# Optimization experiments

Measured on AMD Instinct MI355X. Metric: run time of the kernel, lower is better.

The kernel has to match this reference:

```python
import jax, jax.numpy as jnp
import numpy as np

H = 16
D_MODEL = 1024
D_K = D_MODEL // H
B, S = 4, 2048


def setup_inputs() -> dict:
    key = jax.random.key(0)
    ks = jax.random.split(key, 12)
    s = 1.0 / np.sqrt(D_MODEL)
    inp = {
        "q": jax.random.normal(ks[0], (B, S, D_MODEL), jnp.float32),
        "k": jax.random.normal(ks[1], (B, S, D_MODEL), jnp.float32),
        "v": jax.random.normal(ks[2], (B, S, D_MODEL), jnp.float32),
        "mask": jnp.ones((B, S, S), jnp.int32),
        "Wq": jax.random.normal(ks[3], (D_MODEL, D_MODEL), jnp.float32) * s,
        "bq": jnp.zeros((D_MODEL,), jnp.float32),
        "Wk": jax.random.normal(ks[4], (D_MODEL, D_MODEL), jnp.float32) * s,
        "bk": jnp.zeros((D_MODEL,), jnp.float32),
        "Wv": jax.random.normal(ks[5], (D_MODEL, D_MODEL), jnp.float32) * s,
        "bv": jnp.zeros((D_MODEL,), jnp.float32),
        "Wo": jax.random.normal(ks[6], (D_MODEL, D_MODEL), jnp.float32) * s,
        "bo": jnp.zeros((D_MODEL,), jnp.float32),
    }
    return inp


def _shape_heads(x):
    # [B, S, d_model] -> [B, H, S, d_k]
    b, s, _ = x.shape
    return x.reshape(b, s, H, D_K).transpose(0, 2, 1, 3)


def reference(q, k, v, mask, Wq, bq, Wk, bk, Wv, bv, Wo, bo):
    qh = _shape_heads(q @ Wq + bq)  # [B,H,S,dk]
    kh = _shape_heads(k @ Wk + bk)
    vh = _shape_heads(v @ Wv + bv)
    scores = jnp.einsum("bhqd,bhkd->bhqk", qh, kh) / jnp.sqrt(jnp.float32(D_K))
    scores = jnp.where(mask[:, None, :, :] == 0, jnp.float32(-1e9), scores)
    attn = jax.nn.softmax(scores, axis=-1)  # dropout = identity (eval)
    ctx = jnp.einsum("bhqk,bhkd->bhqd", attn, vh)
    concat = ctx.transpose(0, 2, 1, 3).reshape(q.shape[0], -1, D_MODEL)
    output = concat @ Wo + bo
    return output, attn
```

## Files before the change

kernel.cpp:

```cpp
#include <hip/hip_runtime.h>

#define NH     16
#define SEQ    2048
#define DMODEL 1024
#define DK     64
#define NB     4

typedef __attribute__((ext_vector_type(8))) short short8v;
typedef __attribute__((ext_vector_type(4))) short short4v;
typedef __attribute__((ext_vector_type(4))) float f32x4;

#define EXP_SC 0.18033688011f

__device__ __forceinline__ short f2bf(float x) {
  unsigned u = __float_as_uint(x);
  unsigned r = (u + 0x7FFFu + ((u >> 16) & 1u)) >> 16;
  return (short)r;
}
__device__ __forceinline__ float bf2f(short b) {
  return __uint_as_float(((unsigned)(unsigned short)b) << 16);
}

typedef const __attribute__((address_space(1))) unsigned int* gas_t;
typedef __attribute__((address_space(3))) unsigned int* las_t;
__device__ __forceinline__ void glds16(const void* g, void* l) {
  __builtin_amdgcn_global_load_lds((gas_t)g, (las_t)l, 16, 0, 0);
}

__device__ __forceinline__ void stage_tile(const void* grow0, int gpitchB,
                                           void* ltile, int wid, int lane) {
#pragma unroll
  for (int i = 0; i < 2; ++i) {
    const int row = i * 32 + wid * 8 + (lane >> 3);
    const int srccol = ((lane & 7) * 16) ^ ((lane >> 3) << 4);
    const char* src = reinterpret_cast<const char*>(grow0) + (size_t)row * gpitchB + srccol;
    char* dst = reinterpret_cast<char*>(ltile) + i * 4096 + wid * 1024;
    glds16(src, dst);
  }
}

__device__ __forceinline__ short8v ldfrag(const short* base, int row, int colByte) {
  return *reinterpret_cast<const short8v*>(
      reinterpret_cast<const char*>(base) + row * 128 + (colByte ^ ((row & 7) << 4)));
}
__device__ __forceinline__ void st8b(short* base, int row, int colByte, short4v v) {
  *reinterpret_cast<short4v*>(
      reinterpret_cast<char*>(base) + row * 128 + (colByte ^ ((row & 7) << 4))) = v;
}

__device__ __forceinline__ void stPf4(float* base, int row, int colByte, float4 v) {
  *reinterpret_cast<float4*>(
      reinterpret_cast<char*>(base) + row * 256 + (colByte ^ ((row & 7) << 4))) = v;
}
__device__ __forceinline__ float4 ldPf4(const float* base, int row, int colByte) {
  return *reinterpret_cast<const float4*>(
      reinterpret_cast<const char*>(base) + row * 256 + (colByte ^ ((row & 7) << 4)));
}

__global__ __launch_bounds__(256) void pack_mask_kernel(
    const int* __restrict__ mask, unsigned long long* __restrict__ bits)
{
  const int t = threadIdx.x;
  const size_t chunk = (size_t)blockIdx.x * 4 + (t >> 6);
  const int lane = t & 63;
  const int m = mask[chunk * 64 + lane];
  const unsigned long long b = __ballot(m != 0);
  if (lane == 0) bits[chunk] = b;
}

__global__ __launch_bounds__(256) void convert_f32_bf16_kernel(
    const float* __restrict__ in, short* __restrict__ out)
{
  const int idx = blockIdx.x * 256 + threadIdx.x;
  const float4 x0 = *reinterpret_cast<const float4*>(&in[(size_t)idx * 8]);
  const float4 x1 = *reinterpret_cast<const float4*>(&in[(size_t)idx * 8 + 4]);
  short8v o;
  o[0] = f2bf(x0.x); o[1] = f2bf(x0.y); o[2] = f2bf(x0.z); o[3] = f2bf(x0.w);
  o[4] = f2bf(x1.x); o[5] = f2bf(x1.y); o[6] = f2bf(x1.z); o[7] = f2bf(x1.w);
  *reinterpret_cast<short8v*>(&out[(size_t)idx * 8]) = o;
}

__global__ __launch_bounds__(256) void transpose_w_kernel(
    const float* __restrict__ W, short* __restrict__ WT)
{
  __shared__ short T[64][80];
  const int t  = threadIdx.x;
  const int k0 = blockIdx.x * 64;
  const int n0 = blockIdx.y * 64;

  const int kl = t >> 2, nc = (t & 3) * 16;
#pragma unroll
  for (int i = 0; i < 4; ++i) {
    const float4 x = *reinterpret_cast<const float4*>(&W[(size_t)(k0 + kl) * DMODEL + n0 + nc + i * 4]);
    T[nc + i * 4 + 0][kl] = f2bf(x.x);
    T[nc + i * 4 + 1][kl] = f2bf(x.y);
    T[nc + i * 4 + 2][kl] = f2bf(x.z);
    T[nc + i * 4 + 3][kl] = f2bf(x.w);
  }
  __syncthreads();
  const int nl = t >> 2, kc = (t & 3) * 16;
#pragma unroll
  for (int i = 0; i < 2; ++i) {
    const short8v y = *reinterpret_cast<const short8v*>(&T[nl][kc + i * 8]);
    *reinterpret_cast<short8v*>(&WT[(size_t)(n0 + nl) * DMODEL + k0 + kc + i * 8]) = y;
  }
}

__global__ __launch_bounds__(256) void transpose_w_hilo_kernel(
    const float* __restrict__ W, short* __restrict__ WTh, short* __restrict__ WTl)
{
  __shared__ short Th[64][80];
  __shared__ short Tl[64][80];
  const int t  = threadIdx.x;
  const int k0 = blockIdx.x * 64;
  const int n0 = blockIdx.y * 64;

  const int kl = t >> 2, nc = (t & 3) * 16;
#pragma unroll
  for (int i = 0; i < 4; ++i) {
    const float4 x = *reinterpret_cast<const float4*>(&W[(size_t)(k0 + kl) * DMODEL + n0 + nc + i * 4]);
    const float xv[4] = {x.x, x.y, x.z, x.w};
#pragma unroll
    for (int j = 0; j < 4; ++j) {
      const short hi = f2bf(xv[j]);
      const short lo = f2bf(xv[j] - bf2f(hi));
      Th[nc + i * 4 + j][kl] = hi;
      Tl[nc + i * 4 + j][kl] = lo;
    }
  }
  __syncthreads();
  const int nl = t >> 2, kc = (t & 3) * 16;
#pragma unroll
  for (int i = 0; i < 2; ++i) {
    const short8v yh = *reinterpret_cast<const short8v*>(&Th[nl][kc + i * 8]);
    const short8v yl = *reinterpret_cast<const short8v*>(&Tl[nl][kc + i * 8]);
    *reinterpret_cast<short8v*>(&WTh[(size_t)(n0 + nl) * DMODEL + k0 + kc + i * 8]) = yh;
    *reinterpret_cast<short8v*>(&WTl[(size_t)(n0 + nl) * DMODEL + k0 + kc + i * 8]) = yl;
  }
}

__global__ __launch_bounds__(256) void proj_mfma_kernel(
    const short* __restrict__ A,
    const short* __restrict__ BT,
    const float* __restrict__ bias,
    short* __restrict__ out)
{
  __shared__ short As[128 * 64];
  __shared__ short Bs[128 * 64];

  const int t = threadIdx.x, lane = t & 63, wid = t >> 6;
  const int g = lane >> 4, r15 = lane & 15;
  const int m0 = blockIdx.x * 128, n0 = blockIdx.y * 128;
  const int wm = (wid >> 1) * 64, wn = (wid & 1) * 64;

  f32x4 acc[4][4];
#pragma unroll
  for (int i = 0; i < 4; ++i)
#pragma unroll
    for (int j = 0; j < 4; ++j) acc[i][j] = (f32x4){0.f, 0.f, 0.f, 0.f};

  for (int k0 = 0; k0 < DMODEL; k0 += 64) {
    __syncthreads();
    stage_tile(A + (size_t)m0 * DMODEL + k0, DMODEL * 2, As, wid, lane);
    stage_tile(A + (size_t)(m0 + 64) * DMODEL + k0, DMODEL * 2, As + 64 * 64, wid, lane);
    stage_tile(BT + (size_t)n0 * DMODEL + k0, DMODEL * 2, Bs, wid, lane);
    stage_tile(BT + (size_t)(n0 + 64) * DMODEL + k0, DMODEL * 2, Bs + 64 * 64, wid, lane);
    __syncthreads();

#pragma unroll
    for (int w = 0; w < 2; ++w) {
      short8v a[4], b[4];
#pragma unroll
      for (int i = 0; i < 4; ++i) a[i] = ldfrag(As, wm + i * 16 + r15, w * 64 + g * 16);
#pragma unroll
      for (int j = 0; j < 4; ++j) b[j] = ldfrag(Bs, wn + j * 16 + r15, w * 64 + g * 16);
#pragma unroll
      for (int i = 0; i < 4; ++i)
#pragma unroll
        for (int j = 0; j < 4; ++j)
          acc[i][j] = __builtin_amdgcn_mfma_f32_16x16x32_bf16(a[i], b[j], acc[i][j], 0, 0, 0);
    }
  }

#pragma unroll
  for (int j = 0; j < 4; ++j) {
    const int n = n0 + wn + j * 16 + r15;
    const int hh = n >> 6, dd = n & 63;
    const float bv = bias[n];
#pragma unroll
    for (int i = 0; i < 4; ++i) {
#pragma unroll
      for (int reg = 0; reg < 4; ++reg) {
        const int m = m0 + wm + i * 16 + g * 4 + reg;
        const int bb = m >> 11, ss = m & 2047;
        out[((size_t)(bb * NH + hh) * SEQ + ss) * DK + dd] = f2bf(acc[i][j][reg] + bv);
      }
    }
  }
}

__global__ __launch_bounds__(256) void outproj_mfma_kernel(
    const short* __restrict__ Ahp, const short* __restrict__ Alp,
    const short* __restrict__ BTh, const short* __restrict__ BTl,
    const float* __restrict__ bias, float* __restrict__ out)
{
  __shared__ short Ah[128 * 64];
  __shared__ short Al[128 * 64];
  __shared__ short Bh[128 * 64];
  __shared__ short Bl[128 * 64];

  const int t = threadIdx.x, lane = t & 63, wid = t >> 6;
  const int g = lane >> 4, r15 = lane & 15;
  const int m0 = blockIdx.x * 128, n0 = blockIdx.y * 128;
  const int wm = (wid >> 1) * 64, wn = (wid & 1) * 64;

  f32x4 acc[4][4];
#pragma unroll
  for (int i = 0; i < 4; ++i)
#pragma unroll
    for (int j = 0; j < 4; ++j) acc[i][j] = (f32x4){0.f, 0.f, 0.f, 0.f};

  for (int k0 = 0; k0 < DMODEL; k0 += 64) {
    __syncthreads();
    stage_tile(Ahp + (size_t)m0 * DMODEL + k0, DMODEL * 2, Ah, wid, lane);
    stage_tile(Ahp + (size_t)(m0 + 64) * DMODEL + k0, DMODEL * 2, Ah + 64 * 64, wid, lane);
    stage_tile(Alp + (size_t)m0 * DMODEL + k0, DMODEL * 2, Al, wid, lane);
    stage_tile(Alp + (size_t)(m0 + 64) * DMODEL + k0, DMODEL * 2, Al + 64 * 64, wid, lane);
    stage_tile(BTh + (size_t)n0 * DMODEL + k0, DMODEL * 2, Bh, wid, lane);
    stage_tile(BTh + (size_t)(n0 + 64) * DMODEL + k0, DMODEL * 2, Bh + 64 * 64, wid, lane);
    stage_tile(BTl + (size_t)n0 * DMODEL + k0, DMODEL * 2, Bl, wid, lane);
    stage_tile(BTl + (size_t)(n0 + 64) * DMODEL + k0, DMODEL * 2, Bl + 64 * 64, wid, lane);
    __syncthreads();

#pragma unroll
    for (int w = 0; w < 2; ++w) {
      short8v ah[4], al[4];
#pragma unroll
      for (int i = 0; i < 4; ++i) {
        ah[i] = ldfrag(Ah, wm + i * 16 + r15, w * 64 + g * 16);
        al[i] = ldfrag(Al, wm + i * 16 + r15, w * 64 + g * 16);
      }
#pragma unroll
      for (int j = 0; j < 4; ++j) {
        const short8v bh = ldfrag(Bh, wn + j * 16 + r15, w * 64 + g * 16);
        const short8v bl = ldfrag(Bl, wn + j * 16 + r15, w * 64 + g * 16);
#pragma unroll
        for (int i = 0; i < 4; ++i) {
          acc[i][j] = __builtin_amdgcn_mfma_f32_16x16x32_bf16(ah[i], bh, acc[i][j], 0, 0, 0);
          acc[i][j] = __builtin_amdgcn_mfma_f32_16x16x32_bf16(ah[i], bl, acc[i][j], 0, 0, 0);
          acc[i][j] = __builtin_amdgcn_mfma_f32_16x16x32_bf16(al[i], bh, acc[i][j], 0, 0, 0);
        }
      }
    }
  }

#pragma unroll
  for (int j = 0; j < 4; ++j) {
    const int n = n0 + wn + j * 16 + r15;
    const float bv = bias[n];
#pragma unroll
    for (int i = 0; i < 4; ++i)
#pragma unroll
      for (int reg = 0; reg < 4; ++reg) {
        const int m = m0 + wm + i * 16 + g * 4 + reg;
        out[(size_t)m * DMODEL + n] = acc[i][j][reg] + bv;
      }
  }
}

__global__ __launch_bounds__(256) void transpose_v_kernel(
    const short* __restrict__ vhb, short* __restrict__ vT)
{
  __shared__ short T[64][72];
  const int t    = threadIdx.x;
  const int s0   = blockIdx.x * 64;
  const int head = blockIdx.y;
  const size_t ibase = (size_t)head * SEQ * DK;
  const size_t obase = (size_t)head * DK * SEQ;

  const int sl = t >> 2, d0 = (t & 3) * 16;
#pragma unroll
  for (int i = 0; i < 2; ++i) {
    const short8v x = *reinterpret_cast<const short8v*>(
        &vhb[ibase + (size_t)(s0 + sl) * DK + d0 + i * 8]);
#pragma unroll
    for (int j = 0; j < 8; ++j) T[d0 + i * 8 + j][sl] = x[j];
  }
  __syncthreads();
  const int dl = t >> 2, soff = (t & 3) * 16;
#pragma unroll
  for (int i = 0; i < 2; ++i) {
    const short8v y = *reinterpret_cast<const short8v*>(&T[dl][soff + i * 8]);
    *reinterpret_cast<short8v*>(&vT[obase + (size_t)dl * SEQ + s0 + soff + i * 8]) = y;
  }
}

__global__ __launch_bounds__(256) void flash_kernel(
    const short* __restrict__ qh, const short* __restrict__ kh,
    const short* __restrict__ vT, const unsigned long long* __restrict__ maskbits,
    short* __restrict__ ctxh, short* __restrict__ ctxl,
    float* __restrict__ linv_arr)
{
  __shared__ short Qs[64 * 64];
  __shared__ short Ks[64 * 64];
  __shared__ short VsT[64 * 64];
  __shared__ short Psb[64 * 64];

  const int t    = threadIdx.x;
  const int lane = t & 63;
  const int wid  = t >> 6;
  const int g    = lane >> 4;
  const int r15  = lane & 15;
  const int qbase = wid * 16;
  const int qrow  = qbase + r15;

  const int q0 = blockIdx.x * 64;
  const int h  = blockIdx.y;
  const int b  = blockIdx.z;

  const size_t headbase = ((size_t)(b * NH + h)) * SEQ * DK;
  const size_t vTbase   = ((size_t)(b * NH + h)) * DK * SEQ;
  const size_t mrow     = ((size_t)b * SEQ + (q0 + qrow)) * (SEQ / 64);

  stage_tile(qh + headbase + (size_t)q0 * DK, DK * 2, Qs, wid, lane);
  __syncthreads();

  const short8v bQ0 = ldfrag(Qs, qrow, g * 16);
  const short8v bQ1 = ldfrag(Qs, qrow, 64 + g * 16);

  float lsum = 0.f;
  f32x4 cacc[4];
#pragma unroll
  for (int i = 0; i < 4; ++i) cacc[i] = (f32x4){0.f, 0.f, 0.f, 0.f};

  for (int t64 = 0; t64 < 32; ++t64) {
    __syncthreads();
    stage_tile(kh + headbase + (size_t)t64 * 64 * DK, DK * 2, Ks, wid, lane);
    stage_tile(reinterpret_cast<const char*>(vT + vTbase + t64 * 64), SEQ * 2, VsT, wid, lane);
    __syncthreads();

    f32x4 acc[4];
#pragma unroll
    for (int t4 = 0; t4 < 4; ++t4) acc[t4] = (f32x4){0.f, 0.f, 0.f, 0.f};
#pragma unroll
    for (int t4 = 0; t4 < 4; ++t4) {
      const short8v aK0 = ldfrag(Ks, t4 * 16 + r15, g * 16);
      const short8v aK1 = ldfrag(Ks, t4 * 16 + r15, 64 + g * 16);
      acc[t4] = __builtin_amdgcn_mfma_f32_16x16x32_bf16(aK0, bQ0, acc[t4], 0, 0, 0);
      acc[t4] = __builtin_amdgcn_mfma_f32_16x16x32_bf16(aK1, bQ1, acc[t4], 0, 0, 0);
    }

    const unsigned long long mb = maskbits[mrow + t64];
#pragma unroll
    for (int t4 = 0; t4 < 4; ++t4) {
      const unsigned b4 = (unsigned)(mb >> (t4 * 16 + g * 4)) & 0xFu;
      short4v pk;
#pragma unroll
      for (int reg = 0; reg < 4; ++reg) {
        const float p = ((b4 >> reg) & 1u) ? exp2f(acc[t4][reg] * EXP_SC) : 0.f;
        lsum += p;
        pk[reg] = f2bf(p);
      }
      st8b(Psb, qrow, t4 * 32 + g * 8, pk);
    }

    {
      const short8v aP0 = ldfrag(Psb, qrow, g * 16);
      const short8v aP1 = ldfrag(Psb, qrow, 64 + g * 16);
#pragma unroll
      for (int dt = 0; dt < 4; ++dt) {
        const short8v bV0 = ldfrag(VsT, dt * 16 + r15, g * 16);
        const short8v bV1 = ldfrag(VsT, dt * 16 + r15, 64 + g * 16);
        cacc[dt] = __builtin_amdgcn_mfma_f32_16x16x32_bf16(aP0, bV0, cacc[dt], 0, 0, 0);
        cacc[dt] = __builtin_amdgcn_mfma_f32_16x16x32_bf16(aP1, bV1, cacc[dt], 0, 0, 0);
      }
    }
  }

  float l = lsum;
  l += __shfl_xor(l, 16);
  l += __shfl_xor(l, 32);
  const float linv = 1.0f / l;
  if (g == 0)
    linv_arr[(size_t)(b * NH + h) * SEQ + q0 + qrow] = linv;

  float linvr[4];
#pragma unroll
  for (int reg = 0; reg < 4; ++reg) linvr[reg] = __shfl(linv, g * 4 + reg);

#pragma unroll
  for (int dt = 0; dt < 4; ++dt)
#pragma unroll
    for (int reg = 0; reg < 4; ++reg) {
      const float x = cacc[dt][reg] * linvr[reg];
      const short hi = f2bf(x);
      const short lo = f2bf(x - bf2f(hi));
      const size_t off = (size_t)(b * SEQ + q0 + qbase + g * 4 + reg) * DMODEL
                       + h * DK + dt * 16 + r15;
      ctxh[off] = hi;
      ctxl[off] = lo;
    }
}

__global__ __launch_bounds__(256) void probs_kernel(
    const short* __restrict__ qh, const short* __restrict__ kh,
    const unsigned long long* __restrict__ maskbits,
    const float* __restrict__ linv_arr,
    float* __restrict__ attn_out)
{
  __shared__ short Qs[64 * 64];
  __shared__ short Ks[2][64 * 64];
  __shared__ float PsbF[64 * 64];

  const int t    = threadIdx.x;
  const int lane = t & 63;
  const int wid  = t >> 6;
  const int g    = lane >> 4;
  const int r15  = lane & 15;
  const int qbase = wid * 16;
  const int qrow  = qbase + r15;

  const int q0 = blockIdx.x * 64;
  const int h  = blockIdx.y;
  const int b  = blockIdx.z;

  const size_t headbase = ((size_t)(b * NH + h)) * SEQ * DK;
  const size_t attnbase = ((size_t)(b * NH + h)) * SEQ * SEQ;
  const size_t mrow     = ((size_t)b * SEQ + (q0 + qrow)) * (SEQ / 64);

  const float linv = linv_arr[(size_t)(b * NH + h) * SEQ + q0 + qrow];

  stage_tile(qh + headbase + (size_t)q0 * DK, DK * 2, Qs, wid, lane);
  stage_tile(kh + headbase, DK * 2, Ks[0], wid, lane);
  asm volatile("s_waitcnt vmcnt(0)" ::: "memory");
  __builtin_amdgcn_s_barrier();

  const short8v bQ0 = ldfrag(Qs, qrow, g * 16);
  const short8v bQ1 = ldfrag(Qs, qrow, 64 + g * 16);

  for (int t64 = 0; t64 < 32; ++t64) {
    const int cur = t64 & 1;
    if (t64 + 1 < 32)
      stage_tile(kh + headbase + (size_t)(t64 + 1) * 64 * DK, DK * 2,
                 Ks[cur ^ 1], wid, lane);
    __builtin_amdgcn_sched_barrier(0);

    f32x4 acc[4];
#pragma unroll
    for (int t4 = 0; t4 < 4; ++t4) acc[t4] = (f32x4){0.f, 0.f, 0.f, 0.f};
#pragma unroll
    for (int t4 = 0; t4 < 4; ++t4) {
      const short8v aK0 = ldfrag(Ks[cur], t4 * 16 + r15, g * 16);
      const short8v aK1 = ldfrag(Ks[cur], t4 * 16 + r15, 64 + g * 16);
      acc[t4] = __builtin_amdgcn_mfma_f32_16x16x32_bf16(aK0, bQ0, acc[t4], 0, 0, 0);
      acc[t4] = __builtin_amdgcn_mfma_f32_16x16x32_bf16(aK1, bQ1, acc[t4], 0, 0, 0);
    }

    const unsigned long long mb = maskbits[mrow + t64];
#pragma unroll
    for (int t4 = 0; t4 < 4; ++t4) {
      const unsigned b4 = (unsigned)(mb >> (t4 * 16 + g * 4)) & 0xFu;
      float4 pv;
      pv.x = (b4 & 1u) ? exp2f(acc[t4][0] * EXP_SC) * linv : 0.f;
      pv.y = (b4 & 2u) ? exp2f(acc[t4][1] * EXP_SC) * linv : 0.f;
      pv.z = (b4 & 4u) ? exp2f(acc[t4][2] * EXP_SC) * linv : 0.f;
      pv.w = (b4 & 8u) ? exp2f(acc[t4][3] * EXP_SC) * linv : 0.f;
      stPf4(PsbF, qrow, t4 * 64 + g * 16, pv);
    }

#pragma unroll
    for (int i = 0; i < 4; ++i) {
      const int prow = qbase + i * 4 + g;
      const float4 f = ldPf4(PsbF, prow, r15 * 16);
      *reinterpret_cast<float4*>(
          &attn_out[attnbase + (size_t)(q0 + prow) * SEQ + t64 * 64 + r15 * 4]) = f;
    }

    asm volatile("s_waitcnt vmcnt(4)" ::: "memory");
    __builtin_amdgcn_s_barrier();
  }
}


extern "C" void kernel_launch(void* const* d_in, const int* in_sizes, int n_in,
                              void* d_out, int out_size, void* d_ws, size_t ws_size,
                              hipStream_t stream) {
  const float* q    = (const float*)d_in[0];
  const float* k    = (const float*)d_in[1];
  const float* v    = (const float*)d_in[2];
  const int*   mask = (const int*)d_in[3];
  const float* Wq   = (const float*)d_in[4];
  const float* bq   = (const float*)d_in[5];
  const float* Wk   = (const float*)d_in[6];
  const float* bk   = (const float*)d_in[7];
  const float* Wv   = (const float*)d_in[8];
  const float* bv   = (const float*)d_in[9];
  const float* Wo   = (const float*)d_in[10];
  const float* bo   = (const float*)d_in[11];

  float* out  = (float*)d_out;
  float* attn = out + (size_t)NB * SEQ * DMODEL;

  const size_t HSZ = (size_t)NB * NH * SEQ * DK;
  const size_t WSZ = (size_t)DMODEL * DMODEL;
  short* qhb  = (short*)d_ws;
  short* khb  = qhb + HSZ;
  short* vhb  = khb + HSZ;
  short* Xbuf = vhb + HSZ;
  short* vTb  = Xbuf + HSZ;
  short* WTq  = vTb + HSZ;
  short* WTk  = WTq + WSZ;
  short* WTv  = WTk + WSZ;
  short* WToh = WTv + WSZ;
  short* WTol = WToh + WSZ;
  unsigned long long* maskbits = (unsigned long long*)(WTol + WSZ);
  float* linv_arr = (float*)(maskbits + (size_t)NB * SEQ * (SEQ / 64));
  short* ctxh = vhb;
  short* ctxl = Xbuf;

  const dim3 blk(256);

  pack_mask_kernel<<<dim3((NB * SEQ * SEQ / 64) / 4), blk, 0, stream>>>(mask, maskbits);

  const dim3 gwt(16, 16);
  transpose_w_kernel<<<gwt, blk, 0, stream>>>(Wq, WTq);
  transpose_w_kernel<<<gwt, blk, 0, stream>>>(Wk, WTk);
  transpose_w_kernel<<<gwt, blk, 0, stream>>>(Wv, WTv);
  transpose_w_hilo_kernel<<<gwt, blk, 0, stream>>>(Wo, WToh, WTol);

  const int nconv = (int)(NB * SEQ * DMODEL / 8 / 256);
  const dim3 gproj(64, 8);

  convert_f32_bf16_kernel<<<nconv, blk, 0, stream>>>(q, Xbuf);
  proj_mfma_kernel<<<gproj, blk, 0, stream>>>(Xbuf, WTq, bq, qhb);
  convert_f32_bf16_kernel<<<nconv, blk, 0, stream>>>(k, Xbuf);
  proj_mfma_kernel<<<gproj, blk, 0, stream>>>(Xbuf, WTk, bk, khb);
  convert_f32_bf16_kernel<<<nconv, blk, 0, stream>>>(v, Xbuf);
  proj_mfma_kernel<<<gproj, blk, 0, stream>>>(Xbuf, WTv, bv, vhb);

  transpose_v_kernel<<<dim3(SEQ / 64, NB * NH), blk, 0, stream>>>(vhb, vTb);

  const dim3 gattn(SEQ / 64, NH, NB);
  flash_kernel<<<gattn, blk, 0, stream>>>(qhb, khb, vTb, maskbits,
                                          ctxh, ctxl, linv_arr);
  probs_kernel<<<gattn, blk, 0, stream>>>(qhb, khb, maskbits, linv_arr, attn);

  outproj_mfma_kernel<<<gproj, blk, 0, stream>>>(ctxh, ctxl, WToh, WTol, bo, out);
}
```

Baseline: 628.0 us.

## Double-buffer LDS tiles in projection, out-projection and flash kernels

Converts the K-loop tile staging in the projection GEMM, the split-bf16 out-projection GEMM and the flash attention kernel to double-buffered LDS. The next tile's global-to-LDS loads are issued before computing on the current tile, and each iteration ends with one waitcnt plus barrier instead of two syncthreads. The out-projection also moves to 32-wide K tiles with a new swizzle to keep its LDS footprint at the previous size while doubling buffers. This hides global load latency behind MFMA work, at the cost of more LDS in the projection and flash kernels, which may lower occupancy.

```diff
diff --git a/kernel.cpp b/kernel.cpp
--- a/kernel.cpp
+++ b/kernel.cpp
@@ -39,6 +39,18 @@
   }
 }
 
+__device__ __forceinline__ void stage_tile32(const void* grow0, int gpitchB,
+                                             void* ltile, int wid, int lane) {
+#pragma unroll
+  for (int half = 0; half < 2; ++half) {
+    const int row = half * 64 + wid * 16 + (lane >> 2);
+    const int srccol = ((lane & 3) * 16) ^ (((lane >> 3) & 3) << 4);
+    const char* src = reinterpret_cast<const char*>(grow0) + (size_t)row * gpitchB + srccol;
+    char* dst = reinterpret_cast<char*>(ltile) + half * 4096 + wid * 1024;
+    glds16(src, dst);
+  }
+}
+
 __device__ __forceinline__ short8v ldfrag(const short* base, int row, int colByte) {
   return *reinterpret_cast<const short8v*>(
       reinterpret_cast<const char*>(base) + row * 128 + (colByte ^ ((row & 7) << 4)));
@@ -46,6 +58,10 @@
 __device__ __forceinline__ void st8b(short* base, int row, int colByte, short4v v) {
   *reinterpret_cast<short4v*>(
       reinterpret_cast<char*>(base) + row * 128 + (colByte ^ ((row & 7) << 4))) = v;
+}
+__device__ __forceinline__ short8v ldfrag32(const short* base, int row, int colByte) {
+  return *reinterpret_cast<const short8v*>(
+      reinterpret_cast<const char*>(base) + row * 64 + (colByte ^ (((row >> 1) & 3) << 4)));
 }
 
 __device__ __forceinline__ void stPf4(float* base, int row, int colByte, float4 v) {
@@ -145,8 +161,8 @@
     const float* __restrict__ bias,
     short* __restrict__ out)
 {
-  __shared__ short As[128 * 64];
-  __shared__ short Bs[128 * 64];
+  __shared__ short As[2][128 * 64];
+  __shared__ short Bs[2][128 * 64];
 
   const int t = threadIdx.x, lane = t & 63, wid = t >> 6;
   const int g = lane >> 4, r15 = lane & 15;
@@ -159,27 +175,40 @@
 #pragma unroll
     for (int j = 0; j < 4; ++j) acc[i][j] = (f32x4){0.f, 0.f, 0.f, 0.f};
 
-  for (int k0 = 0; k0 < DMODEL; k0 += 64) {
-    __syncthreads();
-    stage_tile(A + (size_t)m0 * DMODEL + k0, DMODEL * 2, As, wid, lane);
-    stage_tile(A + (size_t)(m0 + 64) * DMODEL + k0, DMODEL * 2, As + 64 * 64, wid, lane);
-    stage_tile(BT + (size_t)n0 * DMODEL + k0, DMODEL * 2, Bs, wid, lane);
-    stage_tile(BT + (size_t)(n0 + 64) * DMODEL + k0, DMODEL * 2, Bs + 64 * 64, wid, lane);
-    __syncthreads();
+  stage_tile(A + (size_t)m0 * DMODEL, DMODEL * 2, As[0], wid, lane);
+  stage_tile(A + (size_t)(m0 + 64) * DMODEL, DMODEL * 2, As[0] + 64 * 64, wid, lane);
+  stage_tile(BT + (size_t)n0 * DMODEL, DMODEL * 2, Bs[0], wid, lane);
+  stage_tile(BT + (size_t)(n0 + 64) * DMODEL, DMODEL * 2, Bs[0] + 64 * 64, wid, lane);
+  asm volatile("s_waitcnt vmcnt(0)" ::: "memory");
+  __builtin_amdgcn_s_barrier();
+
+  for (int kt = 0; kt < 16; ++kt) {
+    const int cur = kt & 1;
+    if (kt < 15) {
+      const int k0 = (kt + 1) * 64;
+      stage_tile(A + (size_t)m0 * DMODEL + k0, DMODEL * 2, As[cur ^ 1], wid, lane);
+      stage_tile(A + (size_t)(m0 + 64) * DMODEL + k0, DMODEL * 2, As[cur ^ 1] + 64 * 64, wid, lane);
+      stage_tile(BT + (size_t)n0 * DMODEL + k0, DMODEL * 2, Bs[cur ^ 1], wid, lane);
+      stage_tile(BT + (size_t)(n0 + 64) * DMODEL + k0, DMODEL * 2, Bs[cur ^ 1] + 64 * 64, wid, lane);
+    }
+    __builtin_amdgcn_sched_barrier(0);
 
 #pragma unroll
     for (int w = 0; w < 2; ++w) {
       short8v a[4], b[4];
 #pragma unroll
-      for (int i = 0; i < 4; ++i) a[i] = ldfrag(As, wm + i * 16 + r15, w * 64 + g * 16);
-#pragma unroll
-      for (int j = 0; j < 4; ++j) b[j] = ldfrag(Bs, wn + j * 16 + r15, w * 64 + g * 16);
+      for (int i = 0; i < 4; ++i) a[i] = ldfrag(As[cur], wm + i * 16 + r15, w * 64 + g * 16);
+#pragma unroll
+      for (int j = 0; j < 4; ++j) b[j] = ldfrag(Bs[cur], wn + j * 16 + r15, w * 64 + g * 16);
 #pragma unroll
       for (int i = 0; i < 4; ++i)
 #pragma unroll
         for (int j = 0; j < 4; ++j)
           acc[i][j] = __builtin_amdgcn_mfma_f32_16x16x32_bf16(a[i], b[j], acc[i][j], 0, 0, 0);
     }
+
+    asm volatile("s_waitcnt vmcnt(0)" ::: "memory");
+    __builtin_amdgcn_s_barrier();
   }
 
 #pragma unroll
@@ -204,10 +233,10 @@
     const short* __restrict__ BTh, const short* __restrict__ BTl,
     const float* __restrict__ bias, float* __restrict__ out)
 {
-  __shared__ short Ah[128 * 64];
-  __shared__ short Al[128 * 64];
-  __shared__ short Bh[128 * 64];
-  __shared__ short Bl[128 * 64];
+  __shared__ short Ah[2][128 * 32];
+  __shared__ short Al[2][128 * 32];
+  __shared__ short Bh[2][128 * 32];
+  __shared__ short Bl[2][128 * 32];
 
   const int t = threadIdx.x, lane = t & 63, wid = t >> 6;
   const int g = lane >> 4, r15 = lane & 15;
@@ -220,38 +249,47 @@
 #pragma unroll
     for (int j = 0; j < 4; ++j) acc[i][j] = (f32x4){0.f, 0.f, 0.f, 0.f};
 
-  for (int k0 = 0; k0 < DMODEL; k0 += 64) {
-    __syncthreads();
-    stage_tile(Ahp + (size_t)m0 * DMODEL + k0, DMODEL * 2, Ah, wid, lane);
-    stage_tile(Ahp + (size_t)(m0 + 64) * DMODEL + k0, DMODEL * 2, Ah + 64 * 64, wid, lane);
-    stage_tile(Alp + (size_t)m0 * DMODEL + k0, DMODEL * 2, Al, wid, lane);
-    stage_tile(Alp + (size_t)(m0 + 64) * DMODEL + k0, DMODEL * 2, Al + 64 * 64, wid, lane);
-    stage_tile(BTh + (size_t)n0 * DMODEL + k0, DMODEL * 2, Bh, wid, lane);
-    stage_tile(BTh + (size_t)(n0 + 64) * DMODEL + k0, DMODEL * 2, Bh + 64 * 64, wid, lane);
-    stage_tile(BTl + (size_t)n0 * DMODEL + k0, DMODEL * 2, Bl, wid, lane);
-    stage_tile(BTl + (size_t)(n0 + 64) * DMODEL + k0, DMODEL * 2, Bl + 64 * 64, wid, lane);
-    __syncthreads();
-
-#pragma unroll
-    for (int w = 0; w < 2; ++w) {
-      short8v ah[4], al[4];
+  const size_t abase = (size_t)m0 * DMODEL;
+  const size_t bbase = (size_t)n0 * DMODEL;
+
+  stage_tile32(Ahp + abase, DMODEL * 2, Ah[0], wid, lane);
+  stage_tile32(Alp + abase, DMODEL * 2, Al[0], wid, lane);
+  stage_tile32(BTh + bbase, DMODEL * 2, Bh[0], wid, lane);
+  stage_tile32(BTl + bbase, DMODEL * 2, Bl[0], wid, lane);
+  asm volatile("s_waitcnt vmcnt(0)" ::: "memory");
+  __builtin_amdgcn_s_barrier();
+
+  for (int kt = 0; kt < 32; ++kt) {
+    const int cur = kt & 1;
+    if (kt < 31) {
+      const int k0 = (kt + 1) * 32;
+      stage_tile32(Ahp + abase + k0, DMODEL * 2, Ah[cur ^ 1], wid, lane);
+      stage_tile32(Alp + abase + k0, DMODEL * 2, Al[cur ^ 1], wid, lane);
+      stage_tile32(BTh + bbase + k0, DMODEL * 2, Bh[cur ^ 1], wid, lane);
+      stage_tile32(BTl + bbase + k0, DMODEL * 2, Bl[cur ^ 1], wid, lane);
+    }
+    __builtin_amdgcn_sched_barrier(0);
+
+    short8v ah[4], al[4];
+#pragma unroll
+    for (int i = 0; i < 4; ++i) {
+      ah[i] = ldfrag32(Ah[cur], wm + i * 16 + r15, g * 16);
+      al[i] = ldfrag32(Al[cur], wm + i * 16 + r15, g * 16);
+    }
+#pragma unroll
+    for (int j = 0; j < 4; ++j) {
+      const short8v bh = ldfrag32(Bh[cur], wn + j * 16 + r15, g * 16);
+      const short8v bl = ldfrag32(Bl[cur], wn + j * 16 + r15, g * 16);
 #pragma unroll
       for (int i = 0; i < 4; ++i) {
-        ah[i] = ldfrag(Ah, wm + i * 16 + r15, w * 64 + g * 16);
-        al[i] = ldfrag(Al, wm + i * 16 + r15, w * 64 + g * 16);
+        acc[i][j] = __builtin_amdgcn_mfma_f32_16x16x32_bf16(ah[i], bh, acc[i][j], 0, 0, 0);
+        acc[i][j] = __builtin_amdgcn_mfma_f32_16x16x32_bf16(ah[i], bl, acc[i][j], 0, 0, 0);
+        acc[i][j] = __builtin_amdgcn_mfma_f32_16x16x32_bf16(al[i], bh, acc[i][j], 0, 0, 0);
       }
-#pragma unroll
-      for (int j = 0; j < 4; ++j) {
-        const short8v bh = ldfrag(Bh, wn + j * 16 + r15, w * 64 + g * 16);
-        const short8v bl = ldfrag(Bl, wn + j * 16 + r15, w * 64 + g * 16);
-#pragma unroll
-        for (int i = 0; i < 4; ++i) {
-          acc[i][j] = __builtin_amdgcn_mfma_f32_16x16x32_bf16(ah[i], bh, acc[i][j], 0, 0, 0);
-          acc[i][j] = __builtin_amdgcn_mfma_f32_16x16x32_bf16(ah[i], bl, acc[i][j], 0, 0, 0);
-          acc[i][j] = __builtin_amdgcn_mfma_f32_16x16x32_bf16(al[i], bh, acc[i][j], 0, 0, 0);
-        }
-      }
-    }
+    }
+
+    asm volatile("s_waitcnt vmcnt(0)" ::: "memory");
+    __builtin_amdgcn_s_barrier();
   }
 
 #pragma unroll
@@ -302,8 +340,8 @@
     float* __restrict__ linv_arr)
 {
   __shared__ short Qs[64 * 64];
-  __shared__ short Ks[64 * 64];
-  __shared__ short VsT[64 * 64];
+  __shared__ short Ks[2][64 * 64];
+  __shared__ short VsT[2][64 * 64];
   __shared__ short Psb[64 * 64];
 
   const int t    = threadIdx.x;
@@ -323,7 +361,10 @@
   const size_t mrow     = ((size_t)b * SEQ + (q0 + qrow)) * (SEQ / 64);
 
   stage_tile(qh + headbase + (size_t)q0 * DK, DK * 2, Qs, wid, lane);
-  __syncthreads();
+  stage_tile(kh + headbase, DK * 2, Ks[0], wid, lane);
+  stage_tile(reinterpret_cast<const char*>(vT + vTbase), SEQ * 2, VsT[0], wid, lane);
+  asm volatile("s_waitcnt vmcnt(0)" ::: "memory");
+  __builtin_amdgcn_s_barrier();
 
   const short8v bQ0 = ldfrag(Qs, qrow, g * 16);
   const short8v bQ1 = ldfrag(Qs, qrow, 64 + g * 16);
@@ -334,18 +375,21 @@
   for (int i = 0; i < 4; ++i) cacc[i] = (f32x4){0.f, 0.f, 0.f, 0.f};
 
   for (int t64 = 0; t64 < 32; ++t64) {
-    __syncthreads();
-    stage_tile(kh + headbase + (size_t)t64 * 64 * DK, DK * 2, Ks, wid, lane);
-    stage_tile(reinterpret_cast<const char*>(vT + vTbase + t64 * 64), SEQ * 2, VsT, wid, lane);
-    __syncthreads();
+    const int cur = t64 & 1;
+    if (t64 < 31) {
+      stage_tile(kh + headbase + (size_t)(t64 + 1) * 64 * DK, DK * 2, Ks[cur ^ 1], wid, lane);
+      stage_tile(reinterpret_cast<const char*>(vT + vTbase + (t64 + 1) * 64), SEQ * 2,
+                 VsT[cur ^ 1], wid, lane);
+    }
+    __builtin_amdgcn_sched_barrier(0);
 
     f32x4 acc[4];
 #pragma unroll
     for (int t4 = 0; t4 < 4; ++t4) acc[t4] = (f32x4){0.f, 0.f, 0.f, 0.f};
 #pragma unroll
     for (int t4 = 0; t4 < 4; ++t4) {
-      const short8v aK0 = ldfrag(Ks, t4 * 16 + r15, g * 16);
-      const short8v aK1 = ldfrag(Ks, t4 * 16 + r15, 64 + g * 16);
+      const short8v aK0 = ldfrag(Ks[cur], t4 * 16 + r15, g * 16);
+      const short8v aK1 = ldfrag(Ks[cur], t4 * 16 + r15, 64 + g * 16);
       acc[t4] = __builtin_amdgcn_mfma_f32_16x16x32_bf16(aK0, bQ0, acc[t4], 0, 0, 0);
       acc[t4] = __builtin_amdgcn_mfma_f32_16x16x32_bf16(aK1, bQ1, acc[t4], 0, 0, 0);
     }
@@ -369,12 +413,15 @@
       const short8v aP1 = ldfrag(Psb, qrow, 64 + g * 16);
 #pragma unroll
       for (int dt = 0; dt < 4; ++dt) {
-        const short8v bV0 = ldfrag(VsT, dt * 16 + r15, g * 16);
-        const short8v bV1 = ldfrag(VsT, dt * 16 + r15, 64 + g * 16);
+        const short8v bV0 = ldfrag(VsT[cur], dt * 16 + r15, g * 16);
+        const short8v bV1 = ldfrag(VsT[cur], dt * 16 + r15, 64 + g * 16);
         cacc[dt] = __builtin_amdgcn_mfma_f32_16x16x32_bf16(aP0, bV0, cacc[dt], 0, 0, 0);
         cacc[dt] = __builtin_amdgcn_mfma_f32_16x16x32_bf16(aP1, bV1, cacc[dt], 0, 0, 0);
       }
     }
+
+    asm volatile("s_waitcnt vmcnt(0)" ::: "memory");
+    __builtin_amdgcn_s_barrier();
   }
 
   float l = lsum;
```

Result: slower. 647.0 us (+3.0%).

## Use 128-query tiles with 8 waves, double-buffer K/V, swizzle blocks, nontemporal attn stores

Applied to the files above, without the earlier changes.

Flash and probs kernels now run 512 threads per block covering 128 query rows, so each K/V tile staged in shared memory serves twice as many queries. The flash kernel adds double-buffered K and V^T tiles with prefetch of the next tile and a single barrier per iteration. Block indices are remapped through a 1D swizzle that spreads consecutive blocks across heads and batches, and attention-probability stores become nontemporal to avoid polluting cache. The cost is more LDS per block and fewer blocks overall, which may reduce occupancy.

```diff
diff --git a/kernel.cpp b/kernel.cpp
--- a/kernel.cpp
+++ b/kernel.cpp
@@ -35,6 +35,26 @@
     const int srccol = ((lane & 7) * 16) ^ ((lane >> 3) << 4);
     const char* src = reinterpret_cast<const char*>(grow0) + (size_t)row * gpitchB + srccol;
     char* dst = reinterpret_cast<char*>(ltile) + i * 4096 + wid * 1024;
+    glds16(src, dst);
+  }
+}
+
+__device__ __forceinline__ void stage_tile_h8(const void* grow0, int gpitchB,
+                                              void* ltile, int wid, int lane) {
+  const int row = wid * 8 + (lane >> 3);
+  const int srccol = ((lane & 7) * 16) ^ ((lane >> 3) << 4);
+  const char* src = reinterpret_cast<const char*>(grow0) + (size_t)row * gpitchB + srccol;
+  char* dst = reinterpret_cast<char*>(ltile) + wid * 1024;
+  glds16(src, dst);
+}
+__device__ __forceinline__ void stage_tile128(const void* grow0, int gpitchB,
+                                              void* ltile, int wid, int lane) {
+#pragma unroll
+  for (int i = 0; i < 2; ++i) {
+    const int row = i * 64 + wid * 8 + (lane >> 3);
+    const int srccol = ((lane & 7) * 16) ^ ((lane >> 3) << 4);
+    const char* src = reinterpret_cast<const char*>(grow0) + (size_t)row * gpitchB + srccol;
+    char* dst = reinterpret_cast<char*>(ltile) + i * 8192 + wid * 1024;
     glds16(src, dst);
   }
 }
@@ -295,16 +315,16 @@
   }
 }
 
-__global__ __launch_bounds__(256) void flash_kernel(
+__global__ __launch_bounds__(512) void flash_kernel(
     const short* __restrict__ qh, const short* __restrict__ kh,
     const short* __restrict__ vT, const unsigned long long* __restrict__ maskbits,
     short* __restrict__ ctxh, short* __restrict__ ctxl,
     float* __restrict__ linv_arr)
 {
-  __shared__ short Qs[64 * 64];
-  __shared__ short Ks[64 * 64];
-  __shared__ short VsT[64 * 64];
-  __shared__ short Psb[64 * 64];
+  __shared__ short Qs[128 * 64];
+  __shared__ short Ks[2][64 * 64];
+  __shared__ short VsT[2][64 * 64];
+  __shared__ short Psb[128 * 64];
 
   const int t    = threadIdx.x;
   const int lane = t & 63;
@@ -314,16 +334,22 @@
   const int qbase = wid * 16;
   const int qrow  = qbase + r15;
 
-  const int q0 = blockIdx.x * 64;
-  const int h  = blockIdx.y;
-  const int b  = blockIdx.z;
+  const int bid = blockIdx.x;
+  const int swz = (bid & 7) * 128 + (bid >> 3);
+  const int qt = swz & 15;
+  const int h  = (swz >> 4) & 15;
+  const int b  = swz >> 8;
+  const int q0 = qt * 128;
 
   const size_t headbase = ((size_t)(b * NH + h)) * SEQ * DK;
   const size_t vTbase   = ((size_t)(b * NH + h)) * DK * SEQ;
   const size_t mrow     = ((size_t)b * SEQ + (q0 + qrow)) * (SEQ / 64);
 
-  stage_tile(qh + headbase + (size_t)q0 * DK, DK * 2, Qs, wid, lane);
-  __syncthreads();
+  stage_tile128(qh + headbase + (size_t)q0 * DK, DK * 2, Qs, wid, lane);
+  stage_tile_h8(kh + headbase, DK * 2, Ks[0], wid, lane);
+  stage_tile_h8(reinterpret_cast<const char*>(vT + vTbase), SEQ * 2, VsT[0], wid, lane);
+  asm volatile("s_waitcnt vmcnt(0)" ::: "memory");
+  __builtin_amdgcn_s_barrier();
 
   const short8v bQ0 = ldfrag(Qs, qrow, g * 16);
   const short8v bQ1 = ldfrag(Qs, qrow, 64 + g * 16);
@@ -334,18 +360,22 @@
   for (int i = 0; i < 4; ++i) cacc[i] = (f32x4){0.f, 0.f, 0.f, 0.f};
 
   for (int t64 = 0; t64 < 32; ++t64) {
-    __syncthreads();
-    stage_tile(kh + headbase + (size_t)t64 * 64 * DK, DK * 2, Ks, wid, lane);
-    stage_tile(reinterpret_cast<const char*>(vT + vTbase + t64 * 64), SEQ * 2, VsT, wid, lane);
-    __syncthreads();
+    const int cur = t64 & 1;
+    if (t64 < 31) {
+      stage_tile_h8(kh + headbase + (size_t)(t64 + 1) * 64 * DK, DK * 2,
+                    Ks[cur ^ 1], wid, lane);
+      stage_tile_h8(reinterpret_cast<const char*>(vT + vTbase + (t64 + 1) * 64), SEQ * 2,
+                    VsT[cur ^ 1], wid, lane);
+    }
+    __builtin_amdgcn_sched_barrier(0);
 
     f32x4 acc[4];
 #pragma unroll
     for (int t4 = 0; t4 < 4; ++t4) acc[t4] = (f32x4){0.f, 0.f, 0.f, 0.f};
 #pragma unroll
     for (int t4 = 0; t4 < 4; ++t4) {
-      const short8v aK0 = ldfrag(Ks, t4 * 16 + r15, g * 16);
-      const short8v aK1 = ldfrag(Ks, t4 * 16 + r15, 64 + g * 16);
+      const short8v aK0 = ldfrag(Ks[cur], t4 * 16 + r15, g * 16);
+      const short8v aK1 = ldfrag(Ks[cur], t4 * 16 + r15, 64 + g * 16);
       acc[t4] = __builtin_amdgcn_mfma_f32_16x16x32_bf16(aK0, bQ0, acc[t4], 0, 0, 0);
       acc[t4] = __builtin_amdgcn_mfma_f32_16x16x32_bf16(aK1, bQ1, acc[t4], 0, 0, 0);
     }
@@ -369,12 +399,15 @@
       const short8v aP1 = ldfrag(Psb, qrow, 64 + g * 16);
 #pragma unroll
       for (int dt = 0; dt < 4; ++dt) {
-        const short8v bV0 = ldfrag(VsT, dt * 16 + r15, g * 16);
-        const short8v bV1 = ldfrag(VsT, dt * 16 + r15, 64 + g * 16);
+        const short8v bV0 = ldfrag(VsT[cur], dt * 16 + r15, g * 16);
+        const short8v bV1 = ldfrag(VsT[cur], dt * 16 + r15, 64 + g * 16);
         cacc[dt] = __builtin_amdgcn_mfma_f32_16x16x32_bf16(aP0, bV0, cacc[dt], 0, 0, 0);
         cacc[dt] = __builtin_amdgcn_mfma_f32_16x16x32_bf16(aP1, bV1, cacc[dt], 0, 0, 0);
       }
     }
+
+    asm volatile("s_waitcnt vmcnt(0)" ::: "memory");
+    __builtin_amdgcn_s_barrier();
   }
 
   float l = lsum;
@@ -402,15 +435,15 @@
     }
 }
 
-__global__ __launch_bounds__(256) void probs_kernel(
+__global__ __launch_bounds__(512) void probs_kernel(
     const short* __restrict__ qh, const short* __restrict__ kh,
     const unsigned long long* __restrict__ maskbits,
     const float* __restrict__ linv_arr,
     float* __restrict__ attn_out)
 {
-  __shared__ short Qs[64 * 64];
+  __shared__ short Qs[128 * 64];
   __shared__ short Ks[2][64 * 64];
-  __shared__ float PsbF[64 * 64];
+  __shared__ float PsbF[128 * 64];
 
   const int t    = threadIdx.x;
   const int lane = t & 63;
@@ -420,9 +453,12 @@
   const int qbase = wid * 16;
   const int qrow  = qbase + r15;
 
-  const int q0 = blockIdx.x * 64;
-  const int h  = blockIdx.y;
-  const int b  = blockIdx.z;
+  const int bid = blockIdx.x;
+  const int swz = (bid & 7) * 128 + (bid >> 3);
+  const int qt = swz & 15;
+  const int h  = (swz >> 4) & 15;
+  const int b  = swz >> 8;
+  const int q0 = qt * 128;
 
   const size_t headbase = ((size_t)(b * NH + h)) * SEQ * DK;
   const size_t attnbase = ((size_t)(b * NH + h)) * SEQ * SEQ;
@@ -430,8 +466,8 @@
 
   const float linv = linv_arr[(size_t)(b * NH + h) * SEQ + q0 + qrow];
 
-  stage_tile(qh + headbase + (size_t)q0 * DK, DK * 2, Qs, wid, lane);
-  stage_tile(kh + headbase, DK * 2, Ks[0], wid, lane);
+  stage_tile128(qh + headbase + (size_t)q0 * DK, DK * 2, Qs, wid, lane);
+  stage_tile_h8(kh + headbase, DK * 2, Ks[0], wid, lane);
   asm volatile("s_waitcnt vmcnt(0)" ::: "memory");
   __builtin_amdgcn_s_barrier();
 
@@ -441,8 +477,8 @@
   for (int t64 = 0; t64 < 32; ++t64) {
     const int cur = t64 & 1;
     if (t64 + 1 < 32)
-      stage_tile(kh + headbase + (size_t)(t64 + 1) * 64 * DK, DK * 2,
-                 Ks[cur ^ 1], wid, lane);
+      stage_tile_h8(kh + headbase + (size_t)(t64 + 1) * 64 * DK, DK * 2,
+                    Ks[cur ^ 1], wid, lane);
     __builtin_amdgcn_sched_barrier(0);
 
     f32x4 acc[4];
@@ -472,8 +508,9 @@
     for (int i = 0; i < 4; ++i) {
       const int prow = qbase + i * 4 + g;
       const float4 f = ldPf4(PsbF, prow, r15 * 16);
-      *reinterpret_cast<float4*>(
-          &attn_out[attnbase + (size_t)(q0 + prow) * SEQ + t64 * 64 + r15 * 4]) = f;
+      f32x4 fv; fv[0] = f.x; fv[1] = f.y; fv[2] = f.z; fv[3] = f.w;
+      __builtin_nontemporal_store(fv, reinterpret_cast<f32x4*>(
+          &attn_out[attnbase + (size_t)(q0 + prow) * SEQ + t64 * 64 + r15 * 4]));
     }
 
     asm volatile("s_waitcnt vmcnt(4)" ::: "memory");
@@ -519,6 +556,7 @@
   short* ctxl = Xbuf;
 
   const dim3 blk(256);
+  const dim3 blk8(512);
 
   pack_mask_kernel<<<dim3((NB * SEQ * SEQ / 64) / 4), blk, 0, stream>>>(mask, maskbits);
 
@@ -540,10 +578,10 @@
 
   transpose_v_kernel<<<dim3(SEQ / 64, NB * NH), blk, 0, stream>>>(vhb, vTb);
 
-  const dim3 gattn(SEQ / 64, NH, NB);
-  flash_kernel<<<gattn, blk, 0, stream>>>(qhb, khb, vTb, maskbits,
-                                          ctxh, ctxl, linv_arr);
-  probs_kernel<<<gattn, blk, 0, stream>>>(qhb, khb, maskbits, linv_arr, attn);
+  const int nattn = (SEQ / 128) * NH * NB;
+  flash_kernel<<<nattn, blk8, 0, stream>>>(qhb, khb, vTb, maskbits,
+                                           ctxh, ctxl, linv_arr);
+  probs_kernel<<<nattn, blk8, 0, stream>>>(qhb, khb, maskbits, linv_arr, attn);
 
   outproj_mfma_kernel<<<gproj, blk, 0, stream>>>(ctxh, ctxl, WToh, WTol, bo, out);
 }
```

After: 543.4 us. 1.16x faster.
